# Performance work log

Hardware: AMD Instinct MI355X
Metric: run time of the kernel (lower is better)

## Reference

```python
import jax, jax.numpy as jnp
import numpy as np
import math

B, S, D, H, DK, DFF = 64, 512, 512, 8, 64, 2048


def _layernorm(x, g, b, eps=1e-5):
    mu = jnp.mean(x, axis=-1, keepdims=True)
    var = jnp.var(x, axis=-1, keepdims=True)
    return (x - mu) * jax.lax.rsqrt(var + eps) * g + b


def setup_inputs() -> dict:
    key = jax.random.key(0)
    ks = jax.random.split(key, 16)
    std = 0.02
    return {
        "query": jax.random.normal(ks[0], (B, S, D), jnp.float32),
        "key": jax.random.normal(ks[1], (B, S, D), jnp.float32),
        "values": jax.random.normal(ks[2], (B, S, D), jnp.float32),
        "forget_rate": jax.random.uniform(ks[3], (B, 1, S, 1), jnp.float32),
        "Wq": jax.random.normal(ks[4], (D, D), jnp.float32) * std,
        "bq": jnp.zeros((D,), jnp.float32),
        "Wk": jax.random.normal(ks[5], (D, D), jnp.float32) * std,
        "bk": jnp.zeros((D,), jnp.float32),
        "Wv": jax.random.normal(ks[6], (D, D), jnp.float32) * std,
        "bv": jnp.zeros((D,), jnp.float32),
        "Wo": jax.random.normal(ks[7], (D, D), jnp.float32) * std,
        "bo": jnp.zeros((D,), jnp.float32),
        "g1": jnp.ones((D,), jnp.float32),
        "beta1": jnp.zeros((D,), jnp.float32),
        "W1": jax.random.normal(ks[8], (D, DFF), jnp.float32) * std,
        "bf1": jnp.zeros((DFF,), jnp.float32),
        "W2": jax.random.normal(ks[9], (DFF, D), jnp.float32) * std,
        "bf2": jnp.zeros((D,), jnp.float32),
        "g2": jnp.ones((D,), jnp.float32),
        "beta2": jnp.zeros((D,), jnp.float32),
        "mask": 0,
    }


def reference(query, key, values, forget_rate, Wq, bq, Wk, bk, Wv, bv, Wo, bo,
              g1, beta1, W1, bf1, W2, bf2, g2, beta2, mask):
    bs, seqlen, _ = query.shape
    # project and split heads -> [B, H, S, DK]
    q = (query @ Wq + bq).reshape(bs, seqlen, H, DK).transpose(0, 2, 1, 3)
    k = (key @ Wk + bk).reshape(bs, seqlen, H, DK).transpose(0, 2, 1, 3)
    v = (values @ Wv + bv).reshape(bs, seqlen, H, DK).transpose(0, 2, 1, 3)

    scores = jnp.einsum('bhqd,bhkd->bhqk', q, k) / math.sqrt(DK)  # [B,H,S,S]
    # forget_rate [B,1,S,1] broadcasts over heads and key dim (== repeat in torch)
    scores = scores * forget_rate
    # src_mask: allowed where triu(ones, k=mask) == 0, i.e. j < i + mask
    allowed = jnp.tril(jnp.ones((seqlen, seqlen), bool), mask - 1)
    scores = jnp.where(allowed, scores, jnp.float32(-1e32))
    probs = jax.nn.softmax(scores, axis=-1)
    if mask == 0:  # zero_pad: overwrite first query row with zeros
        probs = probs.at[:, :, 0, :].set(0.0)
    out = jnp.einsum('bhqk,bhkd->bhqd', probs, v)  # [B,H,S,DK]
    concat = out.transpose(0, 2, 1, 3).reshape(bs, seqlen, D)
    attn_out = concat @ Wo + bo

    x = _layernorm(query + attn_out, g1, beta1)
    ff = jax.nn.relu(x @ W1 + bf1) @ W2 + bf2
    x = _layernorm(x + ff, g2, beta2)
    return x
```

## Files before the change

kernel.cpp:

```cpp
#include <hip/hip_runtime.h>
#include <hip/hip_bf16.h>
#include <stdint.h>

typedef __attribute__((ext_vector_type(8))) short short8;
typedef __attribute__((ext_vector_type(8))) unsigned short ushort8;
typedef __attribute__((ext_vector_type(4))) unsigned short ushort4v;
typedef __attribute__((ext_vector_type(4))) float f32x4;

#define DEV static __device__ __forceinline__

constexpr int Bc = 64, Sc = 512, Dc = 512, Hc = 8, DKc = 64, DFc = 2048;
constexpr int Mtot = Bc * Sc;
constexpr int CB   = 16;
constexpr int RC   = CB * Sc;

DEV unsigned short f2b(float f) {
    union { float f; unsigned u; } x; x.f = f;
    unsigned r = x.u + 0x7fffu + ((x.u >> 16) & 1u);
    return (unsigned short)(r >> 16);
}
DEV float b2f(unsigned short u) {
    union { unsigned u; float f; } x; x.u = ((unsigned)u) << 16; return x.f;
}

DEV void gload16(const void* g, void* l) {
    __builtin_amdgcn_global_load_lds(
        (const __attribute__((address_space(1))) void*)g,
        (__attribute__((address_space(3))) void*)l, 16, 0, 0);
}

__global__ void k_cvt(const float* __restrict__ in, unsigned short* __restrict__ out, int n8) {
    int idx = blockIdx.x * 256 + threadIdx.x;
    if (idx >= n8) return;
    const float4* p = (const float4*)(in + (size_t)idx * 8);
    float4 a = p[0], b = p[1];
    ushort8 o;
    o[0] = f2b(a.x); o[1] = f2b(a.y); o[2] = f2b(a.z); o[3] = f2b(a.w);
    o[4] = f2b(b.x); o[5] = f2b(b.y); o[6] = f2b(b.z); o[7] = f2b(b.w);
    *(ushort8*)(out + (size_t)idx * 8) = o;
}

__global__ void k_copy8(const unsigned short* __restrict__ in, unsigned short* __restrict__ out, int n8) {
    int idx = blockIdx.x * 256 + threadIdx.x;
    if (idx >= n8) return;
    *(ushort8*)(out + (size_t)idx * 8) = *(const ushort8*)(in + (size_t)idx * 8);
}

DEV void cvt_w_group(const float* __restrict__ in, unsigned short* __restrict__ out,
                     int K, int N, int li) {
    int n = li % N, kc = li / N;
    ushort8 o;
    #pragma unroll
    for (int j = 0; j < 8; ++j) o[j] = f2b(in[(size_t)(kc * 8 + j) * N + n]);
    *(ushort8*)(out + (size_t)n * K + kc * 8) = o;
}

__global__ void k_cvt_w_all(
    const float* __restrict__ Wq, const float* __restrict__ Wk, const float* __restrict__ Wv,
    const float* __restrict__ Wo, const float* __restrict__ W1, const float* __restrict__ W2,
    unsigned short* __restrict__ Wqt, unsigned short* __restrict__ Wkt,
    unsigned short* __restrict__ Wvt, unsigned short* __restrict__ Wot,
    unsigned short* __restrict__ W1t, unsigned short* __restrict__ W2t) {
    int idx = blockIdx.x * 256 + threadIdx.x;
    if (idx < 131072) {
        int w = idx >> 15, r = idx & 32767;
        const float* ins[4] = {Wq, Wk, Wv, Wo};
        unsigned short* outs[4] = {Wqt, Wkt, Wvt, Wot};
        cvt_w_group(ins[w], outs[w], 512, 512, r);
    } else if (idx < 262144) {
        cvt_w_group(W1, W1t, 512, 2048, idx - 131072);
    } else {
        cvt_w_group(W2, W2t, 2048, 512, idx - 262144);
    }
}

__global__ void k_cvt_all(
    const float* __restrict__ Wq, const float* __restrict__ Wk, const float* __restrict__ Wv,
    const float* __restrict__ Wo, const float* __restrict__ W1, const float* __restrict__ W2,
    unsigned short* __restrict__ Wqt, unsigned short* __restrict__ Wkt,
    unsigned short* __restrict__ Wvt, unsigned short* __restrict__ Wot,
    unsigned short* __restrict__ W1t, unsigned short* __restrict__ W2t,
    const float* __restrict__ q_in, const float* __restrict__ k_in, const float* __restrict__ v_in,
    unsigned short* __restrict__ q_out, unsigned short* __restrict__ k_out,
    unsigned short* __restrict__ v_out) {
    int idx = blockIdx.x * 256 + threadIdx.x;
    if (idx >= 393216) {
        int a = idx - 393216;
        const float* in; unsigned short* out; int li;
        if (a < 2097152)       { in = q_in; out = q_out; li = a; }
        else if (a < 4194304)  { in = k_in; out = k_out; li = a - 2097152; }
        else                   { in = v_in; out = v_out; li = a - 4194304; }
        const float4* p = (const float4*)(in + (size_t)li * 8);
        float4 x = p[0], y = p[1];
        ushort8 o;
        o[0] = f2b(x.x); o[1] = f2b(x.y); o[2] = f2b(x.z); o[3] = f2b(x.w);
        o[4] = f2b(y.x); o[5] = f2b(y.y); o[6] = f2b(y.z); o[7] = f2b(y.w);
        *(ushort8*)(out + (size_t)li * 8) = o;
        return;
    }
    if (idx < 131072) {
        int w = idx >> 15, r = idx & 32767;
        const float* ins[4] = {Wq, Wk, Wv, Wo};
        unsigned short* outs[4] = {Wqt, Wkt, Wvt, Wot};
        cvt_w_group(ins[w], outs[w], 512, 512, r);
    } else if (idx < 262144) {
        cvt_w_group(W1, W1t, 512, 2048, idx - 131072);
    } else {
        cvt_w_group(W2, W2t, 2048, 512, idx - 262144);
    }
}

template<int BM, int BN>
DEV void gemm_core(const unsigned short* __restrict__ A, int lda,
                   const unsigned short* __restrict__ Bt, int ldb, int K,
                   unsigned short* lA, unsigned short* lB,
                   f32x4 (&acc)[BM / 32][BN / 32]) {
    constexpr int MF = BM / 32, NF = BN / 32;
    const int tid = threadIdx.x, lane = tid & 63, wv = tid >> 6;
    const int wr = wv >> 1, wc = wv & 1;
    const int l15 = lane & 15, l4 = lane >> 4, l7 = l15 & 7;
    #pragma unroll
    for (int mf = 0; mf < MF; ++mf)
        #pragma unroll
        for (int nf = 0; nf < NF; ++nf)
            acc[mf][nf] = f32x4{0.f, 0.f, 0.f, 0.f};

    auto stage = [&](int buf, int kt0) {
        unsigned short* dA = lA + (size_t)buf * BM * 64;
        #pragma unroll
        for (int r = 0; r < BM / 32; ++r) {
            int c = r * 256 + tid, row = c >> 3, gs = c & 7;
            gload16(A + (size_t)row * lda + kt0 + ((gs ^ (row & 7)) * 8),
                    dA + (size_t)(r * 256 + wv * 64) * 8);
        }
        unsigned short* dB = lB + (size_t)buf * BN * 64;
        #pragma unroll
        for (int r = 0; r < BN / 32; ++r) {
            int c = r * 256 + tid, row = c >> 3, gs = c & 7;
            gload16(Bt + (size_t)row * ldb + kt0 + ((gs ^ (row & 7)) * 8),
                    dB + (size_t)(r * 256 + wv * 64) * 8);
        }
    };

    stage(0, 0);
    __syncthreads();
    const int nk = K / 64;
    for (int t = 0; t < nk; ++t) {
        const int buf = t & 1;
        if (t + 1 < nk) stage(buf ^ 1, (t + 1) * 64);
        const unsigned short* cA = lA + (size_t)buf * BM * 64;
        const unsigned short* cB = lB + (size_t)buf * BN * 64;
        #pragma unroll
        for (int kt = 0; kt < 2; ++kt) {
            short8 af[MF], bfr[NF];
            #pragma unroll
            for (int mf = 0; mf < MF; ++mf)
                af[mf] = *(const short8*)&cA[(wr * (BM / 2) + mf * 16 + l15) * 64 +
                                             (((kt * 4 + l4) ^ l7) * 8)];
            #pragma unroll
            for (int nf = 0; nf < NF; ++nf)
                bfr[nf] = *(const short8*)&cB[(wc * (BN / 2) + nf * 16 + l15) * 64 +
                                              (((kt * 4 + l4) ^ l7) * 8)];
            #pragma unroll
            for (int mf = 0; mf < MF; ++mf)
                #pragma unroll
                for (int nf = 0; nf < NF; ++nf)
                    acc[mf][nf] = __builtin_amdgcn_mfma_f32_16x16x32_bf16(af[mf], bfr[nf], acc[mf][nf], 0, 0, 0);
        }
        __syncthreads();
    }
}

__global__ __launch_bounds__(256) void k_gemm_qkv(
    const unsigned short* __restrict__ X, const unsigned short* __restrict__ Wt,
    const float* __restrict__ bias, unsigned short* __restrict__ out, int which) {
    __shared__ unsigned short lA[2 * 128 * 64], lB[2 * 128 * 64];
    int m0 = blockIdx.x * 128, n0 = blockIdx.y * 128;
    f32x4 acc[4][4];
    gemm_core<128, 128>(X + (size_t)m0 * Dc, Dc, Wt + (size_t)n0 * Dc, Dc, Dc, lA, lB, acc);
    const int lane = threadIdx.x & 63, wv = threadIdx.x >> 6;
    const int wr = wv >> 1, wc = wv & 1, l15 = lane & 15, l4 = lane >> 4;
    #pragma unroll
    for (int mf = 0; mf < 4; ++mf) {
        #pragma unroll
        for (int nf = 0; nf < 4; ++nf) {
            int n = n0 + wc * 64 + nf * 16 + l15;
            int h = n >> 6, dk = n & 63;
            float bv = bias[n];
            if (which == 2) {
                int mg = m0 + wr * 64 + mf * 16 + l4 * 4;
                int b = mg >> 9, s = mg & 511;
                ushort4v o;
                #pragma unroll
                for (int r = 0; r < 4; ++r) o[r] = f2b(acc[mf][nf][r] + bv);
                *(ushort4v*)&out[((size_t)(b * Hc + h) * DKc + dk) * Sc + s] = o;
            } else {
                float scale = (which == 0) ? 0.125f : 1.0f;
                #pragma unroll
                for (int r = 0; r < 4; ++r) {
                    int mg = m0 + wr * 64 + mf * 16 + l4 * 4 + r;
                    int b = mg >> 9, s = mg & 511;
                    out[((size_t)(b * Hc + h) * Sc + s) * DKc + dk] = f2b((acc[mf][nf][r] + bv) * scale);
                }
            }
        }
    }
}

__global__ __launch_bounds__(512) void k_flash(
    const unsigned short* __restrict__ Qb, const unsigned short* __restrict__ Kb,
    const unsigned short* __restrict__ Vt, unsigned short* __restrict__ conc,
    const float* __restrict__ fr, const int* __restrict__ maskp, int b_base) {
    __shared__ unsigned short smem[32768];
    const int head = blockIdx.y, bl = head >> 3, h = head & 7;
    const int bg = b_base + bl;
    const int m0 = (Sc / 256 - 1 - blockIdx.x) * 256;
    const int mv = *maskp;
    const int tid = threadIdx.x, lane = tid & 63, w = tid >> 6;
    const int l15 = lane & 15, l4 = lane >> 4;
    const int l7 = l15 & 7;
    const int rw = w * 32;
    unsigned short* lP = smem + 16384;
    constexpr float LOG2E = 1.44269504088896340736f;

    unsigned short* lQ = smem;
    const unsigned short* Qg = Qb + ((size_t)head * Sc + m0) * DKc;
    #pragma unroll
    for (int r = 0; r < 4; ++r) {
        int c = r * 512 + tid, row = c >> 3, gs = c & 7;
        gload16(Qg + (size_t)row * DKc + ((gs ^ (row & 7)) * 8), lQ + (size_t)(r * 512 + w * 64) * 8);
    }
    __syncthreads();
    short8 qf[2][2];
    #pragma unroll
    for (int kt = 0; kt < 2; ++kt)
        #pragma unroll
        for (int mf = 0; mf < 2; ++mf)
            qf[kt][mf] = *(const short8*)&lQ[(rw + mf * 16 + l15) * 64 + (((kt * 4 + l4) ^ l7) * 8)];
    float frr[8];
    #pragma unroll
    for (int mf = 0; mf < 2; ++mf)
        #pragma unroll
        for (int r = 0; r < 4; ++r)
            frr[mf * 4 + r] = fr[(size_t)bg * Sc + m0 + rw + mf * 16 + l4 * 4 + r] * LOG2E;
    __syncthreads();

    f32x4 accO[2][4];
    #pragma unroll
    for (int mf = 0; mf < 2; ++mf)
        #pragma unroll
        for (int nf = 0; nf < 4; ++nf)
            accO[mf][nf] = f32x4{0.f, 0.f, 0.f, 0.f};
    float l_run[8];
    #pragma unroll
    for (int i = 0; i < 8; ++i) l_run[i] = 0.f;

    const unsigned short* Kg0 = Kb + (size_t)head * Sc * DKc;
    const unsigned short* Vg0 = Vt + (size_t)head * DKc * Sc;
    int nc = ((m0 + 254 + mv) >> 6) + 1;
    if (nc > 8) nc = 8;
    if (nc < 1) nc = 1;

    {
        int row = tid >> 3, gs = tid & 7;
        gload16(Kg0 + (size_t)row * DKc + ((gs ^ (row & 7)) * 8), smem + (size_t)(w * 64) * 8);
        gload16(Vg0 + (size_t)row * Sc + ((gs ^ (row & 7)) * 8), smem + 8192 + (size_t)(w * 64) * 8);
    }
    __syncthreads();

    for (int ci = 0; ci < nc; ++ci) {
        const int buf = ci & 1;
        unsigned short* lK = smem + (size_t)buf * 4096;
        unsigned short* lV = smem + 8192 + (size_t)buf * 4096;
        if (ci + 1 < nc) {
            int n1 = (ci + 1) * 64;
            int row = tid >> 3, gs = tid & 7;
            gload16(Kg0 + (size_t)n1 * DKc + (size_t)row * DKc + ((gs ^ (row & 7)) * 8),
                    smem + (size_t)(buf ^ 1) * 4096 + (size_t)(w * 64) * 8);
            gload16(Vg0 + n1 + (size_t)row * Sc + ((gs ^ (row & 7)) * 8),
                    smem + 8192 + (size_t)(buf ^ 1) * 4096 + (size_t)(w * 64) * 8);
        }
        const int n0c = ci * 64;
        short8 bk[4][2];
        #pragma unroll
        for (int j = 0; j < 4; ++j)
            #pragma unroll
            for (int kt = 0; kt < 2; ++kt)
                bk[j][kt] = *(const short8*)&lK[(j * 16 + l15) * 64 + (((kt * 4 + l4) ^ l7) * 8)];
        #pragma unroll
        for (int mf = 0; mf < 2; ++mf) {
            f32x4 sa[4];
            #pragma unroll
            for (int j = 0; j < 4; ++j) sa[j] = f32x4{0.f, 0.f, 0.f, 0.f};
            #pragma unroll
            for (int kt = 0; kt < 2; ++kt)
                #pragma unroll
                for (int j = 0; j < 4; ++j)
                    sa[j] = __builtin_amdgcn_mfma_f32_16x16x32_bf16(qf[kt][mf], bk[j][kt], sa[j], 0, 0, 0);
            #pragma unroll
            for (int r = 0; r < 4; ++r) {
                int rowl = rw + mf * 16 + l4 * 4 + r;
                int rowg = m0 + rowl;
                int prs = rowl & 7;
                float fres = frr[mf * 4 + r];
                float ps = 0.f;
                #pragma unroll
                for (int j = 0; j < 4; ++j) {
                    int colg = n0c + j * 16 + l15;
                    float p = (colg < rowg + mv) ? exp2f(sa[j][r] * fres) : 0.f;
                    ps += p;
                    int gw = j * 2 + (l15 >> 3);
                    lP[rowl * 64 + ((gw ^ prs) * 8) + l7] = f2b(p);
                }
                l_run[mf * 4 + r] += ps;
            }
        }
        #pragma unroll
        for (int kl = 0; kl < 2; ++kl) {
            short8 pa[2];
            #pragma unroll
            for (int mf = 0; mf < 2; ++mf)
                pa[mf] = *(const short8*)&lP[(rw + mf * 16 + l15) * 64 + (((kl * 4 + l4) ^ l7) * 8)];
            #pragma unroll
            for (int nf = 0; nf < 4; ++nf) {
                short8 bv8 = *(const short8*)&lV[(nf * 16 + l15) * 64 + (((kl * 4 + l4) ^ l7) * 8)];
                #pragma unroll
                for (int mf = 0; mf < 2; ++mf)
                    accO[mf][nf] = __builtin_amdgcn_mfma_f32_16x16x32_bf16(pa[mf], bv8, accO[mf][nf], 0, 0, 0);
            }
        }
        __syncthreads();
    }
    #pragma unroll
    for (int mf = 0; mf < 2; ++mf)
        #pragma unroll
        for (int r = 0; r < 4; ++r) {
            int rowg = m0 + rw + mf * 16 + l4 * 4 + r;
            float l = l_run[mf * 4 + r];
            #pragma unroll
            for (int o = 1; o < 16; o <<= 1) l += __shfl_xor(l, o);
            float inv = (rowg + mv > 0) ? 1.0f / l : 0.f;
            #pragma unroll
            for (int nf = 0; nf < 4; ++nf) {
                int dk = nf * 16 + l15;
                conc[((size_t)bg * Sc + rowg) * Dc + h * DKc + dk] = f2b(accO[mf][nf][r] * inv);
            }
        }
}

__global__ __launch_bounds__(256) void k_wo(
    const unsigned short* __restrict__ Cc, const unsigned short* __restrict__ Wot,
    const float* __restrict__ bo, const float* __restrict__ query, float* __restrict__ y) {
    __shared__ unsigned short lA[2 * 128 * 64], lB[2 * 128 * 64];
    int m0 = blockIdx.x * 128, n0 = blockIdx.y * 128;
    f32x4 acc[4][4];
    gemm_core<128, 128>(Cc + (size_t)m0 * Dc, Dc, Wot + (size_t)n0 * Dc, Dc, Dc, lA, lB, acc);
    const int lane = threadIdx.x & 63, wv = threadIdx.x >> 6;
    const int wr = wv >> 1, wc = wv & 1, l15 = lane & 15, l4 = lane >> 4;
    #pragma unroll
    for (int mf = 0; mf < 4; ++mf)
        #pragma unroll
        for (int nf = 0; nf < 4; ++nf) {
            int n = n0 + wc * 64 + nf * 16 + l15;
            float bv = bo[n];
            #pragma unroll
            for (int r = 0; r < 4; ++r) {
                int m = m0 + wr * 64 + mf * 16 + l4 * 4 + r;
                y[(size_t)m * Dc + n] = acc[mf][nf][r] + bv + query[(size_t)m * Dc + n];
            }
        }
}

__global__ __launch_bounds__(256) void k_ff1(
    const unsigned short* __restrict__ X, const unsigned short* __restrict__ W1t,
    const float* __restrict__ b1, unsigned short* __restrict__ hb) {
    __shared__ unsigned short lA[2 * 128 * 64], lB[2 * 128 * 64];
    int m0 = blockIdx.x * 128, n0 = blockIdx.y * 128;
    f32x4 acc[4][4];
    gemm_core<128, 128>(X + (size_t)m0 * Dc, Dc, W1t + (size_t)n0 * Dc, Dc, Dc, lA, lB, acc);
    const int lane = threadIdx.x & 63, wv = threadIdx.x >> 6;
    const int wr = wv >> 1, wc = wv & 1, l15 = lane & 15, l4 = lane >> 4;
    #pragma unroll
    for (int mf = 0; mf < 4; ++mf)
        #pragma unroll
        for (int nf = 0; nf < 4; ++nf) {
            int n = n0 + wc * 64 + nf * 16 + l15;
            float bv = b1[n];
            #pragma unroll
            for (int r = 0; r < 4; ++r) {
                int m = m0 + wr * 64 + mf * 16 + l4 * 4 + r;
                hb[(size_t)m * DFc + n] = f2b(fmaxf(acc[mf][nf][r] + bv, 0.f));
            }
        }
}

__global__ __launch_bounds__(256) void k_ff2b(
    const unsigned short* __restrict__ Hb, const unsigned short* __restrict__ W2t,
    const float* __restrict__ b2, const unsigned short* __restrict__ residb,
    float* __restrict__ y) {
    __shared__ unsigned short lA[2 * 128 * 64], lB[2 * 128 * 64];
    int m0 = blockIdx.x * 128, n0 = blockIdx.y * 128;
    f32x4 acc[4][4];
    gemm_core<128, 128>(Hb + (size_t)m0 * DFc, DFc, W2t + (size_t)n0 * DFc, DFc, DFc, lA, lB, acc);
    const int lane = threadIdx.x & 63, wv = threadIdx.x >> 6;
    const int wr = wv >> 1, wc = wv & 1, l15 = lane & 15, l4 = lane >> 4;
    #pragma unroll
    for (int mf = 0; mf < 4; ++mf)
        #pragma unroll
        for (int nf = 0; nf < 4; ++nf) {
            int n = n0 + wc * 64 + nf * 16 + l15;
            float bv = b2[n];
            #pragma unroll
            for (int r = 0; r < 4; ++r) {
                int m = m0 + wr * 64 + mf * 16 + l4 * 4 + r;
                y[(size_t)m * Dc + n] = acc[mf][nf][r] + bv + b2f(residb[(size_t)m * Dc + n]);
            }
        }
}

__global__ __launch_bounds__(256) void k_ln(
    const float* __restrict__ in, const float* __restrict__ g, const float* __restrict__ be,
    float* __restrict__ outf, unsigned short* __restrict__ outb) {
    int rid = blockIdx.x * 4 + (threadIdx.x >> 6);
    int lane = threadIdx.x & 63;
    const float* row = in + (size_t)rid * Dc;
    float4 a = ((const float4*)row)[lane * 2];
    float4 b = ((const float4*)row)[lane * 2 + 1];
    float x[8] = {a.x, a.y, a.z, a.w, b.x, b.y, b.z, b.w};
    float s = 0.f, ss = 0.f;
    #pragma unroll
    for (int j = 0; j < 8; ++j) { s += x[j]; ss += x[j] * x[j]; }
    #pragma unroll
    for (int o = 1; o < 64; o <<= 1) { s += __shfl_xor(s, o); ss += __shfl_xor(ss, o); }
    float mu = s * (1.f / 512.f);
    float var = ss * (1.f / 512.f) - mu * mu;
    float rs = rsqrtf(var + 1e-5f);
    float4 g0 = ((const float4*)g)[lane * 2], g1v = ((const float4*)g)[lane * 2 + 1];
    float4 e0 = ((const float4*)be)[lane * 2], e1 = ((const float4*)be)[lane * 2 + 1];
    float gg[8] = {g0.x, g0.y, g0.z, g0.w, g1v.x, g1v.y, g1v.z, g1v.w};
    float ee[8] = {e0.x, e0.y, e0.z, e0.w, e1.x, e1.y, e1.z, e1.w};
    float o8[8];
    #pragma unroll
    for (int j = 0; j < 8; ++j) o8[j] = (x[j] - mu) * rs * gg[j] + ee[j];
    if (outf) {
        float4* po = (float4*)(outf + (size_t)rid * Dc);
        float4 w0 = {o8[0], o8[1], o8[2], o8[3]}, w1 = {o8[4], o8[5], o8[6], o8[7]};
        po[lane * 2] = w0; po[lane * 2 + 1] = w1;
    }
    if (outb) {
        ushort8 ob;
        #pragma unroll
        for (int j = 0; j < 8; ++j) ob[j] = f2b(o8[j]);
        *(ushort8*)(outb + (size_t)rid * Dc + lane * 8) = ob;
    }
}

extern "C" void kernel_launch(void* const* d_in, const int* in_sizes, int n_in,
                              void* d_out, int out_size, void* d_ws, size_t ws_size,
                              hipStream_t stream) {
    const float* query = (const float*)d_in[0];
    const float* key_  = (const float*)d_in[1];
    const float* vals  = (const float*)d_in[2];
    const float* fr    = (const float*)d_in[3];
    const float* Wq = (const float*)d_in[4];  const float* bq = (const float*)d_in[5];
    const float* Wk = (const float*)d_in[6];  const float* bk = (const float*)d_in[7];
    const float* Wv = (const float*)d_in[8];  const float* bv = (const float*)d_in[9];
    const float* Wo = (const float*)d_in[10]; const float* bo = (const float*)d_in[11];
    const float* g1 = (const float*)d_in[12]; const float* be1 = (const float*)d_in[13];
    const float* W1 = (const float*)d_in[14]; const float* b1 = (const float*)d_in[15];
    const float* W2 = (const float*)d_in[16]; const float* b2 = (const float*)d_in[17];
    const float* g2 = (const float*)d_in[18]; const float* be2 = (const float*)d_in[19];
    const int* maskp = (const int*)d_in[20];
    float* out = (float*)d_out;

    char* ab = (char*)d_out;
    unsigned short* xb    = (unsigned short*)ab;
    unsigned short* conc  = (unsigned short*)ab;
    unsigned short* x1b   = conc;
    unsigned short* keyst = (unsigned short*)(ab + (size_t)32 * 1048576);
    unsigned short* Qc   = (unsigned short*)(ab + (size_t)32 * 1048576);
    unsigned short* Kc   = (unsigned short*)(ab + (size_t)40 * 1048576);
    unsigned short* Vc   = (unsigned short*)(ab + (size_t)48 * 1048576);
    unsigned short* xst  = (unsigned short*)(ab + (size_t)56 * 1048576);
    float*          xfc  = (float*)(ab + (size_t)32 * 1048576);

    char* ws = (char*)d_ws;
    unsigned short* Wqt = (unsigned short*)ws;
    unsigned short* Wkt = Wqt + 512 * 512;
    unsigned short* Wvt = Wkt + 512 * 512;
    unsigned short* Wot = Wvt + 512 * 512;
    unsigned short* W1t = Wot + 512 * 512;
    unsigned short* W2t = W1t + 2048 * 512;
    char* wend = (char*)(W2t + 512 * 2048);
    size_t wrem = (ws_size > (size_t)(wend - ws)) ? ws_size - (size_t)(wend - ws) : 0;
    const size_t qkvb = (size_t)Mtot * Dc * 2;

    const bool bigpath = (wrem >= 3 * qkvb);

    const float* acts[3] = {query, key_, vals};
    const unsigned short* wt3[3] = {Wqt, Wkt, Wvt};
    const float* bs3[3] = {bq, bk, bv};

    if (bigpath) {
        unsigned short* QbF = (unsigned short*)wend;
        unsigned short* KbF = QbF + qkvb / 2;
        unsigned short* VtF = KbF + qkvb / 2;
        unsigned short* hb     = QbF;
        unsigned short* resid0 = VtF;
        float*          xf     = (float*)KbF;
        const int Mc = 16384;

        k_cvt_all<<<dim3(26112), dim3(256), 0, stream>>>(
            Wq, Wk, Wv, Wo, W1, W2, Wqt, Wkt, Wvt, Wot, W1t, W2t,
            query, key_, vals, xb, keyst, KbF);

        k_gemm_qkv<<<dim3(Mtot / 128, 4), dim3(256), 0, stream>>>(KbF,   Wvt, bv, VtF, 2);
        k_gemm_qkv<<<dim3(Mtot / 128, 4), dim3(256), 0, stream>>>(keyst, Wkt, bk, KbF, 1);
        k_gemm_qkv<<<dim3(Mtot / 128, 4), dim3(256), 0, stream>>>(xb,    Wqt, bq, QbF, 0);

        k_flash<<<dim3(Sc / 256, Bc * Hc), dim3(512), 0, stream>>>(QbF, KbF, VtF, conc, fr, maskp, 0);

        k_wo<<<dim3(Mtot / 128, 4), dim3(256), 0, stream>>>(conc, Wot, bo, query, xf);
        k_ln<<<dim3(Mtot / 4), dim3(256), 0, stream>>>(xf, g1, be1, (float*)nullptr, x1b);

        k_copy8<<<dim3(Mc / 4), dim3(256), 0, stream>>>(x1b, resid0, Mc * Dc / 8);

        for (int mb = Mtot - Mc; mb >= 0; mb -= Mc) {
            k_ff1<<<dim3(Mc / 128, 16), dim3(256), 0, stream>>>(x1b + (size_t)mb * Dc, W1t, b1, hb);
            k_ff2b<<<dim3(Mc / 128, 4), dim3(256), 0, stream>>>(hb, W2t, b2,
                                                                mb ? x1b + (size_t)mb * Dc : resid0,
                                                                out + (size_t)mb * Dc);
            k_ln<<<dim3(Mc / 4), dim3(256), 0, stream>>>(out + (size_t)mb * Dc, g2, be2,
                                                         out + (size_t)mb * Dc, (unsigned short*)nullptr);
        }
    } else {
        int Mc = 128;
        for (int c = 8192; c >= 128; c >>= 1)
            if ((size_t)c * 5120 <= wrem) { Mc = c; break; }
        unsigned short* hb     = (unsigned short*)wend;
        unsigned short* resid0 = (unsigned short*)(wend + (size_t)Mc * 4096);

        k_cvt_w_all<<<dim3(1536), dim3(256), 0, stream>>>(Wq, Wk, Wv, Wo, W1, W2,
                                                          Wqt, Wkt, Wvt, Wot, W1t, W2t);
        unsigned short* out3[3] = {Qc, Kc, Vc};
        for (int cb = 0; cb < Bc / CB; ++cb) {
            for (int p = 0; p < 3; ++p) {
                k_cvt<<<dim3(RC * Dc / 8 / 256), dim3(256), 0, stream>>>(
                    acts[p] + (size_t)cb * RC * Dc, xst, RC * Dc / 8);
                k_gemm_qkv<<<dim3(RC / 128, 4), dim3(256), 0, stream>>>(xst, wt3[p], bs3[p], out3[p], p);
            }
            k_flash<<<dim3(Sc / 256, CB * Hc), dim3(512), 0, stream>>>(Qc, Kc, Vc, conc, fr, maskp, cb * CB);
        }
        for (int hp = 0; hp < 2; ++hp) {
            int mb = hp * 16384;
            k_wo<<<dim3(16384 / 128, 4), dim3(256), 0, stream>>>(conc + (size_t)mb * Dc, Wot, bo,
                                                                 query + (size_t)mb * Dc, xfc);
            k_ln<<<dim3(16384 / 4), dim3(256), 0, stream>>>(xfc, g1, be1, (float*)nullptr,
                                                            x1b + (size_t)mb * Dc);
        }
        k_copy8<<<dim3(Mc / 4), dim3(256), 0, stream>>>(x1b, resid0, Mc * Dc / 8);
        for (int mb = Mtot - Mc; mb >= 0; mb -= Mc) {
            k_ff1<<<dim3(Mc / 128, 16), dim3(256), 0, stream>>>(x1b + (size_t)mb * Dc, W1t, b1, hb);
            k_ff2b<<<dim3(Mc / 128, 4), dim3(256), 0, stream>>>(hb, W2t, b2,
                                                                mb ? x1b + (size_t)mb * Dc : resid0,
                                                                out + (size_t)mb * Dc);
            k_ln<<<dim3(Mc / 4), dim3(256), 0, stream>>>(out + (size_t)mb * Dc, g2, be2,
                                                         out + (size_t)mb * Dc, (unsigned short*)nullptr);
        }
    }
}
```

Measured before the change: 567.3 us.

## Merge QKV GEMMs into one launch and store pre-LayerNorm sums as bf16

```diff
diff --git a/kernel.cpp b/kernel.cpp
--- a/kernel.cpp
+++ b/kernel.cpp
@@ -171,13 +171,8 @@
     }
 }
 
-__global__ __launch_bounds__(256) void k_gemm_qkv(
-    const unsigned short* __restrict__ X, const unsigned short* __restrict__ Wt,
-    const float* __restrict__ bias, unsigned short* __restrict__ out, int which) {
-    __shared__ unsigned short lA[2 * 128 * 64], lB[2 * 128 * 64];
-    int m0 = blockIdx.x * 128, n0 = blockIdx.y * 128;
-    f32x4 acc[4][4];
-    gemm_core<128, 128>(X + (size_t)m0 * Dc, Dc, Wt + (size_t)n0 * Dc, Dc, Dc, lA, lB, acc);
+DEV void qkv_epilogue(f32x4 (&acc)[4][4], const float* __restrict__ bias,
+                      unsigned short* __restrict__ out, int which, int m0, int n0) {
     const int lane = threadIdx.x & 63, wv = threadIdx.x >> 6;
     const int wr = wv >> 1, wc = wv & 1, l15 = lane & 15, l4 = lane >> 4;
     #pragma unroll
@@ -207,6 +202,36 @@
     }
 }
 
+__global__ __launch_bounds__(256) void k_gemm_qkv(
+    const unsigned short* __restrict__ X, const unsigned short* __restrict__ Wt,
+    const float* __restrict__ bias, unsigned short* __restrict__ out, int which) {
+    __shared__ unsigned short lA[2 * 128 * 64], lB[2 * 128 * 64];
+    int m0 = blockIdx.x * 128, n0 = blockIdx.y * 128;
+    f32x4 acc[4][4];
+    gemm_core<128, 128>(X + (size_t)m0 * Dc, Dc, Wt + (size_t)n0 * Dc, Dc, Dc, lA, lB, acc);
+    qkv_epilogue(acc, bias, out, which, m0, n0);
+}
+
+__global__ __launch_bounds__(256) void k_gemm_qkv3(
+    const unsigned short* __restrict__ Aq, const unsigned short* __restrict__ Ak,
+    const unsigned short* __restrict__ Av,
+    const unsigned short* __restrict__ Wqt, const unsigned short* __restrict__ Wkt,
+    const unsigned short* __restrict__ Wvt,
+    const float* __restrict__ bq, const float* __restrict__ bk, const float* __restrict__ bv,
+    unsigned short* __restrict__ oq, unsigned short* __restrict__ ok,
+    unsigned short* __restrict__ ov) {
+    __shared__ unsigned short lA[2 * 128 * 64], lB[2 * 128 * 64];
+    const int which = blockIdx.z;
+    const unsigned short* X  = which == 0 ? Aq  : (which == 1 ? Ak  : Av);
+    const unsigned short* Wt = which == 0 ? Wqt : (which == 1 ? Wkt : Wvt);
+    const float* bias        = which == 0 ? bq  : (which == 1 ? bk  : bv);
+    unsigned short* out      = which == 0 ? oq  : (which == 1 ? ok  : ov);
+    int m0 = blockIdx.x * 128, n0 = blockIdx.y * 128;
+    f32x4 acc[4][4];
+    gemm_core<128, 128>(X + (size_t)m0 * Dc, Dc, Wt + (size_t)n0 * Dc, Dc, Dc, lA, lB, acc);
+    qkv_epilogue(acc, bias, out, which, m0, n0);
+}
+
 __global__ __launch_bounds__(512) void k_flash(
     const unsigned short* __restrict__ Qb, const unsigned short* __restrict__ Kb,
     const unsigned short* __restrict__ Vt, unsigned short* __restrict__ conc,
@@ -350,7 +375,8 @@
 
 __global__ __launch_bounds__(256) void k_wo(
     const unsigned short* __restrict__ Cc, const unsigned short* __restrict__ Wot,
-    const float* __restrict__ bo, const float* __restrict__ query, float* __restrict__ y) {
+    const float* __restrict__ bo, const float* __restrict__ query,
+    unsigned short* __restrict__ y) {
     __shared__ unsigned short lA[2 * 128 * 64], lB[2 * 128 * 64];
     int m0 = blockIdx.x * 128, n0 = blockIdx.y * 128;
     f32x4 acc[4][4];
@@ -366,7 +392,7 @@
             #pragma unroll
             for (int r = 0; r < 4; ++r) {
                 int m = m0 + wr * 64 + mf * 16 + l4 * 4 + r;
-                y[(size_t)m * Dc + n] = acc[mf][nf][r] + bv + query[(size_t)m * Dc + n];
+                y[(size_t)m * Dc + n] = f2b(acc[mf][nf][r] + bv + query[(size_t)m * Dc + n]);
             }
         }
 }
@@ -394,10 +420,10 @@
         }
 }
 
-__global__ __launch_bounds__(256) void k_ff2b(
+__global__ __launch_bounds__(256) void k_ff2bb(
     const unsigned short* __restrict__ Hb, const unsigned short* __restrict__ W2t,
     const float* __restrict__ b2, const unsigned short* __restrict__ residb,
-    float* __restrict__ y) {
+    unsigned short* __restrict__ y) {
     __shared__ unsigned short lA[2 * 128 * 64], lB[2 * 128 * 64];
     int m0 = blockIdx.x * 128, n0 = blockIdx.y * 128;
     f32x4 acc[4][4];
@@ -413,20 +439,20 @@
             #pragma unroll
             for (int r = 0; r < 4; ++r) {
                 int m = m0 + wr * 64 + mf * 16 + l4 * 4 + r;
-                y[(size_t)m * Dc + n] = acc[mf][nf][r] + bv + b2f(residb[(size_t)m * Dc + n]);
-            }
-        }
-}
-
-__global__ __launch_bounds__(256) void k_ln(
-    const float* __restrict__ in, const float* __restrict__ g, const float* __restrict__ be,
+                y[(size_t)m * Dc + n] = f2b(acc[mf][nf][r] + bv + b2f(residb[(size_t)m * Dc + n]));
+            }
+        }
+}
+
+__global__ __launch_bounds__(256) void k_lnb(
+    const unsigned short* __restrict__ in, const float* __restrict__ g, const float* __restrict__ be,
     float* __restrict__ outf, unsigned short* __restrict__ outb) {
     int rid = blockIdx.x * 4 + (threadIdx.x >> 6);
     int lane = threadIdx.x & 63;
-    const float* row = in + (size_t)rid * Dc;
-    float4 a = ((const float4*)row)[lane * 2];
-    float4 b = ((const float4*)row)[lane * 2 + 1];
-    float x[8] = {a.x, a.y, a.z, a.w, b.x, b.y, b.z, b.w};
+    ushort8 v = *(const ushort8*)(in + (size_t)rid * Dc + lane * 8);
+    float x[8];
+    #pragma unroll
+    for (int j = 0; j < 8; ++j) x[j] = b2f(v[j]);
     float s = 0.f, ss = 0.f;
     #pragma unroll
     for (int j = 0; j < 8; ++j) { s += x[j]; ss += x[j] * x[j]; }
@@ -482,7 +508,7 @@
     unsigned short* Kc   = (unsigned short*)(ab + (size_t)40 * 1048576);
     unsigned short* Vc   = (unsigned short*)(ab + (size_t)48 * 1048576);
     unsigned short* xst  = (unsigned short*)(ab + (size_t)56 * 1048576);
-    float*          xfc  = (float*)(ab + (size_t)32 * 1048576);
+    unsigned short* xfbc = (unsigned short*)(ab + (size_t)32 * 1048576);
 
     char* ws = (char*)d_ws;
     unsigned short* Wqt = (unsigned short*)ws;
@@ -496,49 +522,61 @@
     const size_t qkvb = (size_t)Mtot * Dc * 2;
 
     const bool bigpath = (wrem >= 3 * qkvb);
+    const bool merged  = (wrem >= 4 * qkvb);
 
     const float* acts[3] = {query, key_, vals};
     const unsigned short* wt3[3] = {Wqt, Wkt, Wvt};
     const float* bs3[3] = {bq, bk, bv};
 
     if (bigpath) {
-        unsigned short* QbF = (unsigned short*)wend;
-        unsigned short* KbF = QbF + qkvb / 2;
-        unsigned short* VtF = KbF + qkvb / 2;
+        unsigned short* QbF   = (unsigned short*)wend;
+        unsigned short* KbF   = QbF + qkvb / 2;
+        unsigned short* VtF   = KbF + qkvb / 2;
+        unsigned short* valst = VtF + qkvb / 2;
         unsigned short* hb     = QbF;
         unsigned short* resid0 = VtF;
-        float*          xf     = (float*)KbF;
+        unsigned short* ybb    = VtF + (size_t)8 * 1048576;
+        unsigned short* xfb    = KbF;
         const int Mc = 16384;
 
-        k_cvt_all<<<dim3(26112), dim3(256), 0, stream>>>(
-            Wq, Wk, Wv, Wo, W1, W2, Wqt, Wkt, Wvt, Wot, W1t, W2t,
-            query, key_, vals, xb, keyst, KbF);
-
-        k_gemm_qkv<<<dim3(Mtot / 128, 4), dim3(256), 0, stream>>>(KbF,   Wvt, bv, VtF, 2);
-        k_gemm_qkv<<<dim3(Mtot / 128, 4), dim3(256), 0, stream>>>(keyst, Wkt, bk, KbF, 1);
-        k_gemm_qkv<<<dim3(Mtot / 128, 4), dim3(256), 0, stream>>>(xb,    Wqt, bq, QbF, 0);
+        if (merged) {
+            k_cvt_all<<<dim3(26112), dim3(256), 0, stream>>>(
+                Wq, Wk, Wv, Wo, W1, W2, Wqt, Wkt, Wvt, Wot, W1t, W2t,
+                query, key_, vals, xb, keyst, valst);
+            k_gemm_qkv3<<<dim3(Mtot / 128, 4, 3), dim3(256), 0, stream>>>(
+                xb, keyst, valst, Wqt, Wkt, Wvt, bq, bk, bv, QbF, KbF, VtF);
+        } else {
+            k_cvt_all<<<dim3(26112), dim3(256), 0, stream>>>(
+                Wq, Wk, Wv, Wo, W1, W2, Wqt, Wkt, Wvt, Wot, W1t, W2t,
+                query, key_, vals, xb, keyst, KbF);
+            k_gemm_qkv<<<dim3(Mtot / 128, 4), dim3(256), 0, stream>>>(KbF,   Wvt, bv, VtF, 2);
+            k_gemm_qkv<<<dim3(Mtot / 128, 4), dim3(256), 0, stream>>>(keyst, Wkt, bk, KbF, 1);
+            k_gemm_qkv<<<dim3(Mtot / 128, 4), dim3(256), 0, stream>>>(xb,    Wqt, bq, QbF, 0);
+        }
 
         k_flash<<<dim3(Sc / 256, Bc * Hc), dim3(512), 0, stream>>>(QbF, KbF, VtF, conc, fr, maskp, 0);
 
-        k_wo<<<dim3(Mtot / 128, 4), dim3(256), 0, stream>>>(conc, Wot, bo, query, xf);
-        k_ln<<<dim3(Mtot / 4), dim3(256), 0, stream>>>(xf, g1, be1, (float*)nullptr, x1b);
+        k_wo<<<dim3(Mtot / 128, 4), dim3(256), 0, stream>>>(conc, Wot, bo, query, xfb);
+        k_lnb<<<dim3(Mtot / 4), dim3(256), 0, stream>>>(xfb, g1, be1, (float*)nullptr, x1b);
 
         k_copy8<<<dim3(Mc / 4), dim3(256), 0, stream>>>(x1b, resid0, Mc * Dc / 8);
 
         for (int mb = Mtot - Mc; mb >= 0; mb -= Mc) {
             k_ff1<<<dim3(Mc / 128, 16), dim3(256), 0, stream>>>(x1b + (size_t)mb * Dc, W1t, b1, hb);
-            k_ff2b<<<dim3(Mc / 128, 4), dim3(256), 0, stream>>>(hb, W2t, b2,
-                                                                mb ? x1b + (size_t)mb * Dc : resid0,
-                                                                out + (size_t)mb * Dc);
-            k_ln<<<dim3(Mc / 4), dim3(256), 0, stream>>>(out + (size_t)mb * Dc, g2, be2,
-                                                         out + (size_t)mb * Dc, (unsigned short*)nullptr);
+            k_ff2bb<<<dim3(Mc / 128, 4), dim3(256), 0, stream>>>(hb, W2t, b2,
+                                                                 mb ? x1b + (size_t)mb * Dc : resid0,
+                                                                 ybb);
+            k_lnb<<<dim3(Mc / 4), dim3(256), 0, stream>>>(ybb, g2, be2,
+                                                          out + (size_t)mb * Dc,
+                                                          (unsigned short*)nullptr);
         }
     } else {
         int Mc = 128;
         for (int c = 8192; c >= 128; c >>= 1)
-            if ((size_t)c * 5120 <= wrem) { Mc = c; break; }
+            if ((size_t)c * 6144 <= wrem) { Mc = c; break; }
         unsigned short* hb     = (unsigned short*)wend;
         unsigned short* resid0 = (unsigned short*)(wend + (size_t)Mc * 4096);
+        unsigned short* ybb    = (unsigned short*)(wend + (size_t)Mc * 5120);
 
         k_cvt_w_all<<<dim3(1536), dim3(256), 0, stream>>>(Wq, Wk, Wv, Wo, W1, W2,
                                                           Wqt, Wkt, Wvt, Wot, W1t, W2t);
@@ -554,18 +592,19 @@
         for (int hp = 0; hp < 2; ++hp) {
             int mb = hp * 16384;
             k_wo<<<dim3(16384 / 128, 4), dim3(256), 0, stream>>>(conc + (size_t)mb * Dc, Wot, bo,
-                                                                 query + (size_t)mb * Dc, xfc);
-            k_ln<<<dim3(16384 / 4), dim3(256), 0, stream>>>(xfc, g1, be1, (float*)nullptr,
-                                                            x1b + (size_t)mb * Dc);
+                                                                 query + (size_t)mb * Dc, xfbc);
+            k_lnb<<<dim3(16384 / 4), dim3(256), 0, stream>>>(xfbc, g1, be1, (float*)nullptr,
+                                                             x1b + (size_t)mb * Dc);
         }
         k_copy8<<<dim3(Mc / 4), dim3(256), 0, stream>>>(x1b, resid0, Mc * Dc / 8);
         for (int mb = Mtot - Mc; mb >= 0; mb -= Mc) {
             k_ff1<<<dim3(Mc / 128, 16), dim3(256), 0, stream>>>(x1b + (size_t)mb * Dc, W1t, b1, hb);
-            k_ff2b<<<dim3(Mc / 128, 4), dim3(256), 0, stream>>>(hb, W2t, b2,
-                                                                mb ? x1b + (size_t)mb * Dc : resid0,
-                                                                out + (size_t)mb * Dc);
-            k_ln<<<dim3(Mc / 4), dim3(256), 0, stream>>>(out + (size_t)mb * Dc, g2, be2,
-                                                         out + (size_t)mb * Dc, (unsigned short*)nullptr);
-        }
-    }
-}
+            k_ff2bb<<<dim3(Mc / 128, 4), dim3(256), 0, stream>>>(hb, W2t, b2,
+                                                                 mb ? x1b + (size_t)mb * Dc : resid0,
+                                                                 ybb);
+            k_lnb<<<dim3(Mc / 4), dim3(256), 0, stream>>>(ybb, g2, be2,
+                                                          out + (size_t)mb * Dc,
+                                                          (unsigned short*)nullptr);
+        }
+    }
+}
```

Result: no change. 558.8 us (-1.5%).
